# Kernel optimization log

Hardware: AMD Instinct MI355X
Metric: run time of the kernel (lower is better)

Reference implementation:

```python
import jax, jax.numpy as jnp
import numpy as np

N_NODES = 50000
N_EDGES = 800000
IN_FEATS = 128
OUT_FEATS = 128


def setup_inputs() -> dict:
    key = jax.random.key(0)
    k_feat, k_src, k_dst, k_w1, k_w2, k_lw = jax.random.split(key, 6)
    feat = jax.random.normal(k_feat, (N_NODES, IN_FEATS), dtype=jnp.float32)
    src_idx = jax.random.randint(k_src, (N_EDGES,), 0, N_NODES, dtype=jnp.int64 if jax.config.jax_enable_x64 else jnp.int32)
    dst_idx = jax.random.randint(k_dst, (N_EDGES,), 0, N_NODES, dtype=jnp.int64 if jax.config.jax_enable_x64 else jnp.int32)
    # xavier-uniform-ish scales
    w1_lim = float(np.sqrt(6.0 / (2 * IN_FEATS + IN_FEATS)))
    w2_lim = float(np.sqrt(6.0 / (IN_FEATS + OUT_FEATS)))
    lw_lim = float(np.sqrt(2.0) * np.sqrt(6.0 / (IN_FEATS + OUT_FEATS)))
    weight1 = jax.random.uniform(k_w1, (2 * IN_FEATS, IN_FEATS), jnp.float32, -w1_lim, w1_lim)
    weight2 = jax.random.uniform(k_w2, (IN_FEATS, OUT_FEATS), jnp.float32, -w2_lim, w2_lim)
    loop_weight = jax.random.uniform(k_lw, (IN_FEATS, OUT_FEATS), jnp.float32, -lw_lim, lw_lim)
    bias = jnp.zeros((OUT_FEATS,), dtype=jnp.float32)
    return {
        "feat": feat,
        "src_idx": src_idx,
        "dst_idx": dst_idx,
        "weight1": weight1,
        "weight2": weight2,
        "loop_weight": loop_weight,
        "bias": bias,
    }


def reference(feat, src_idx, dst_idx, weight1, weight2, loop_weight, bias):
    # Gather per-edge src/dst features and concat: [E, 2*d]
    feat_msg = jnp.concatenate([feat[src_idx], feat[dst_idx]], axis=-1)
    # 2-layer edge MLP: relu(msg @ W1) @ W2 -> [E, out]
    e_msg = jnp.matmul(jax.nn.relu(jnp.matmul(feat_msg, weight1)), weight2)
    # Scatter-sum to destination nodes: [N, out]
    rst = jax.ops.segment_sum(e_msg, dst_idx, num_segments=feat.shape[0])
    # bias + residual loop message
    rst = rst + bias + jnp.matmul(feat, loop_weight)
    return rst
```

## Files before the change

### kernel.cpp

```cpp
#include <hip/hip_runtime.h>

typedef __attribute__((ext_vector_type(8))) unsigned short ushort8v;
typedef __attribute__((ext_vector_type(8))) short short8v;
typedef __attribute__((ext_vector_type(4))) float f32x4;

__device__ inline unsigned short f2bf(float f) {
    union { float f; unsigned u; } v; v.f = f;
    unsigned u = v.u;
    unsigned r = (u + 0x7FFFu + ((u >> 16) & 1u)) >> 16;
    return (unsigned short)r;
}
__device__ inline float bf2f(unsigned short h) {
    union { unsigned u; float f; } v; v.u = ((unsigned)h) << 16;
    return v.f;
}

#define CAP 64

__global__ __launch_bounds__(256) void fused_pre(
    const float* __restrict__ feat, unsigned short* __restrict__ X2, int totalF,
    const float* __restrict__ W1, const float* __restrict__ W2,
    const float* __restrict__ LW,
    unsigned short* __restrict__ W1t, unsigned short* __restrict__ W3t,
    int cvtB) {
    int b = blockIdx.x, t = threadIdx.x;
    if (b < cvtB) {
        int idx = (b * 256 + t) * 4;
        if (idx >= totalF) return;
        float4 v = *(const float4*)(feat + idx);
        int row = idx >> 7, col = idx & 127;
        unsigned short* o = X2 + (size_t)row * 256 + 128 + col;
        *(ushort4*)o = make_ushort4(f2bf(v.x), f2bf(v.y), f2bf(v.z), f2bf(v.w));
    } else {
        int i = (b - cvtB) * 256 + t;
        if (i < 32768) {
            int jj = i >> 7, k = i & 127;
            float v = (jj < 128) ? W1[k * 128 + jj] : W1[(128 + k) * 128 + (jj - 128)];
            W1t[i] = f2bf(v);
        } else {
            int i2 = i - 32768;
            int n = i2 >> 8, k = i2 & 255;
            float v = (k < 128) ? W2[k * 128 + n] : LW[(k - 128) * 128 + n];
            W3t[i2] = f2bf(v);
        }
    }
}

template <bool OUT_BF16>
__device__ void gemm_tile(
    unsigned short* As, unsigned short* Bs,
    const unsigned short* __restrict__ A, int lda,
    const unsigned short* __restrict__ Bt, int ldb, int nRowsB,
    void* __restrict__ Cout, int ldc,
    const float* __restrict__ bias, int M, int K, int m0, int n0) {
    const int tid = threadIdx.x;
    const int lane = tid & 63;
    const int w = tid >> 6;
    const int wr = w >> 1, wc = w & 1;
    const int q = lane >> 4, ln = lane & 15;

    f32x4 acc[4][4];
#pragma unroll
    for (int i = 0; i < 4; i++)
#pragma unroll
        for (int j = 0; j < 4; j++) acc[i][j] = (f32x4)0.f;

    for (int kk = 0; kk < K; kk += 64) {
#pragma unroll
        for (int i = 0; i < 4; i++) {
            int id = i * 256 + tid;
            int r = id >> 3, b = id & 7;
            ushort8v v = (ushort8v)(unsigned short)0;
            int gr = m0 + r;
            if (gr < M) v = *(const ushort8v*)(A + (size_t)gr * lda + kk + b * 8);
            *(ushort8v*)(As + r * 64 + ((b ^ (r & 7)) * 8)) = v;
        }
#pragma unroll
        for (int i = 0; i < 4; i++) {
            int id = i * 256 + tid;
            int r = id >> 3, b = id & 7;
            ushort8v v = (ushort8v)(unsigned short)0;
            int gr = n0 + r;
            if (gr < nRowsB) v = *(const ushort8v*)(Bt + (size_t)gr * ldb + kk + b * 8);
            *(ushort8v*)(Bs + r * 64 + ((b ^ (r & 7)) * 8)) = v;
        }
        __syncthreads();
#pragma unroll
        for (int ks = 0; ks < 2; ks++) {
            short8v af[4], bfv[4];
#pragma unroll
            for (int ti = 0; ti < 4; ti++) {
                int m = wr * 64 + ti * 16 + ln;
                int blk = (ks * 4 + q) ^ (m & 7);
                af[ti] = *(const short8v*)(As + m * 64 + blk * 8);
            }
#pragma unroll
            for (int tj = 0; tj < 4; tj++) {
                int n = wc * 64 + tj * 16 + ln;
                int blk = (ks * 4 + q) ^ (n & 7);
                bfv[tj] = *(const short8v*)(Bs + n * 64 + blk * 8);
            }
#pragma unroll
            for (int ti = 0; ti < 4; ti++)
#pragma unroll
                for (int tj = 0; tj < 4; tj++)
                    acc[ti][tj] = __builtin_amdgcn_mfma_f32_16x16x32_bf16(
                        af[ti], bfv[tj], acc[ti][tj], 0, 0, 0);
        }
        __syncthreads();
    }

#pragma unroll
    for (int ti = 0; ti < 4; ti++) {
        int rowb = m0 + wr * 64 + ti * 16 + q * 4;
#pragma unroll
        for (int tj = 0; tj < 4; tj++) {
            int col = n0 + wc * 64 + tj * 16 + ln;
            f32x4 c = acc[ti][tj];
            float bv = 0.f;
            if (!OUT_BF16 && bias) bv = bias[col];
#pragma unroll
            for (int r = 0; r < 4; r++) {
                int row = rowb + r;
                if (row < M) {
                    if (OUT_BF16)
                        ((unsigned short*)Cout)[(size_t)row * ldc + col] = f2bf(c[r]);
                    else
                        ((float*)Cout)[(size_t)row * ldc + col] = c[r] + bv;
                }
            }
        }
    }
}

__global__ __launch_bounds__(256) void gemm1_scatter(
    const unsigned short* __restrict__ X2feat, const unsigned short* __restrict__ W1t,
    unsigned short* __restrict__ AB,
    const int* __restrict__ src, const int* __restrict__ dst,
    int* __restrict__ cur, int* __restrict__ eSrc,
    int E, int gemmB, int N) {
    __shared__ unsigned short smem[2 * 128 * 64];
    int b = blockIdx.x;
    int half = b >> 1;
    if ((b & 1) == 0) {
        if (half >= gemmB) return;
        int m0 = (half >> 1) * 128, n0 = (half & 1) * 128;
        gemm_tile<true>(smem, smem + 128 * 64, X2feat, 256, W1t, 128, 256,
                        (void*)AB, 256, nullptr, N, 128, m0, n0);
    } else {
        int e = (half * 256 + threadIdx.x) * 4;
        if (e + 3 < E) {
            int4 s4 = *(const int4*)(src + e);
            int4 d4 = *(const int4*)(dst + e);
            int p0 = atomicAdd(&cur[d4.x], 1);
            int p1 = atomicAdd(&cur[d4.y], 1);
            int p2 = atomicAdd(&cur[d4.z], 1);
            int p3 = atomicAdd(&cur[d4.w], 1);
            eSrc[(size_t)d4.x * CAP + min(p0, CAP - 1)] = s4.x;
            eSrc[(size_t)d4.y * CAP + min(p1, CAP - 1)] = s4.y;
            eSrc[(size_t)d4.z * CAP + min(p2, CAP - 1)] = s4.z;
            eSrc[(size_t)d4.w * CAP + min(p3, CAP - 1)] = s4.w;
        } else {
            for (int i = e; i < E && i >= 0; i++) {
                int d = dst[i];
                int pos = atomicAdd(&cur[d], 1);
                eSrc[(size_t)d * CAP + min(pos, CAP - 1)] = src[i];
            }
        }
    }
}

__global__ __launch_bounds__(256) void gather_kernel(
    const unsigned short* __restrict__ AB, const int* __restrict__ cur,
    const int* __restrict__ eSrc,
    unsigned short* __restrict__ X2, int N) {
    int wid = (blockIdx.x * 256 + threadIdx.x) >> 6;
    int lane = threadIdx.x & 63;
    if (wid >= N) return;
    int num = min(cur[wid], CAP);
    size_t start = (size_t)wid * CAP;
    int half = lane >> 5, ln32 = lane & 31;
    ushort4 bv = *(const ushort4*)(AB + (size_t)wid * 256 + 128 + ln32 * 4);
    float b0 = bf2f(bv.x), b1 = bf2f(bv.y), b2 = bf2f(bv.z), b3 = bf2f(bv.w);
    float p0 = 0.f, p1 = 0.f, p2 = 0.f, p3 = 0.f;

    int mySrc = (lane < num) ? eSrc[start + lane] : 0;
    int j = 0;
    for (; j + 8 <= num; j += 8) {
        ushort4 v[4];
#pragma unroll
        for (int u = 0; u < 4; u++) {
            int s = __shfl(mySrc, j + 2 * u + half);
            v[u] = *(const ushort4*)(AB + (size_t)s * 256 + ln32 * 4);
        }
#pragma unroll
        for (int u = 0; u < 4; u++) {
            p0 += fmaxf(bf2f(v[u].x) + b0, 0.f);
            p1 += fmaxf(bf2f(v[u].y) + b1, 0.f);
            p2 += fmaxf(bf2f(v[u].z) + b2, 0.f);
            p3 += fmaxf(bf2f(v[u].w) + b3, 0.f);
        }
    }
    for (; j < num; j += 2) {
        int idx = j + half;
        int s = __shfl(mySrc, idx);
        bool ok = idx < num;
        ushort4 v = *(const ushort4*)(AB + (size_t)s * 256 + ln32 * 4);
        float m = ok ? 1.f : 0.f;
        p0 += m * fmaxf(bf2f(v.x) + b0, 0.f);
        p1 += m * fmaxf(bf2f(v.y) + b1, 0.f);
        p2 += m * fmaxf(bf2f(v.z) + b2, 0.f);
        p3 += m * fmaxf(bf2f(v.w) + b3, 0.f);
    }
    p0 += __shfl_xor(p0, 32);
    p1 += __shfl_xor(p1, 32);
    p2 += __shfl_xor(p2, 32);
    p3 += __shfl_xor(p3, 32);
    if (half == 0) {
        *(ushort4*)(X2 + (size_t)wid * 256 + ln32 * 4) =
            make_ushort4(f2bf(p0), f2bf(p1), f2bf(p2), f2bf(p3));
    }
}

template <bool OUT_BF16>
__global__ __launch_bounds__(256) void gemm128(
    const unsigned short* __restrict__ A, int lda,
    const unsigned short* __restrict__ Bt, int ldb, int nRowsB,
    void* __restrict__ Cout, int ldc,
    const float* __restrict__ bias, int M, int K) {
    __shared__ unsigned short smem[2 * 128 * 64];
    gemm_tile<OUT_BF16>(smem, smem + 128 * 64, A, lda, Bt, ldb, nRowsB,
                        Cout, ldc, bias, M, K, blockIdx.x * 128, blockIdx.y * 128);
}

extern "C" void kernel_launch(void* const* d_in, const int* in_sizes, int n_in,
                              void* d_out, int out_size, void* d_ws, size_t ws_size,
                              hipStream_t stream) {
    const float* feat = (const float*)d_in[0];
    const int* src = (const int*)d_in[1];
    const int* dst = (const int*)d_in[2];
    const float* W1 = (const float*)d_in[3];
    const float* W2 = (const float*)d_in[4];
    const float* LW = (const float*)d_in[5];
    const float* bias = (const float*)d_in[6];
    float* out = (float*)d_out;

    const int N = in_sizes[0] / 128;
    const int E = in_sizes[1];

    char* ws = (char*)d_ws;
    unsigned short* X2 = (unsigned short*)ws;
    size_t off_b = (size_t)N * 256 * 2;
    unsigned short* AB = (unsigned short*)(ws + off_b);
    off_b += (size_t)N * 256 * 2;
    unsigned short* W1t = (unsigned short*)(ws + off_b);
    off_b += (size_t)256 * 128 * 2;
    unsigned short* W3t = (unsigned short*)(ws + off_b);
    off_b += (size_t)128 * 256 * 2;
    int* cur = (int*)(ws + off_b);   off_b += (size_t)N * 4;
    int* eSrc = (int*)(ws + off_b);  off_b += (size_t)N * CAP * 4;

    int totalF = N * 128;
    int cvtB = (totalF / 4 + 255) / 256;

    hipMemsetAsync(cur, 0, (size_t)N * 4, stream);
    fused_pre<<<cvtB + 256, 256, 0, stream>>>(
        feat, X2, totalF, W1, W2, LW, W1t, W3t, cvtB);

    int gemmB = ((N + 127) / 128) * 2;
    int scatB = ((E + 3) / 4 + 255) / 256;
    int mx = gemmB > scatB ? gemmB : scatB;
    gemm1_scatter<<<2 * mx, 256, 0, stream>>>(
        X2 + 128, W1t, AB, src, dst, cur, eSrc, E, gemmB, N);

    gather_kernel<<<(N + 3) / 4, 256, 0, stream>>>(AB, cur, eSrc, X2, N);

    dim3 g2((N + 127) / 128, 1);
    gemm128<false><<<g2, 256, 0, stream>>>(X2, 256, W3t, 256, 128,
                                           (void*)out, 128, bias, N, 256);
}
```

Baseline: 183.7 us.

## Split final GEMM: compute loop residual early, accumulate aggregated half later

The memset of the per-node counter array is folded into the preprocessing kernel as extra zeroing blocks, removing a separate memset launch. The self-loop GEMM (feat @ loop_weight + bias) now runs inside the gemm1/scatter kernel as extra even-indexed blocks, so it overlaps with the edge scatter and the first edge GEMM. The last kernel then does only a K=128 GEMM on the aggregated features and adds into the output with read-modify-write. This halves the K of the final GEMM but adds an extra read of the output and more blocks in the middle kernel.

```diff
diff --git a/kernel.cpp b/kernel.cpp
--- a/kernel.cpp
+++ b/kernel.cpp
@@ -22,7 +22,7 @@
     const float* __restrict__ W1, const float* __restrict__ W2,
     const float* __restrict__ LW,
     unsigned short* __restrict__ W1t, unsigned short* __restrict__ W3t,
-    int cvtB) {
+    int* __restrict__ cur, int N, int cvtB) {
     int b = blockIdx.x, t = threadIdx.x;
     if (b < cvtB) {
         int idx = (b * 256 + t) * 4;
@@ -31,7 +31,7 @@
         int row = idx >> 7, col = idx & 127;
         unsigned short* o = X2 + (size_t)row * 256 + 128 + col;
         *(ushort4*)o = make_ushort4(f2bf(v.x), f2bf(v.y), f2bf(v.z), f2bf(v.w));
-    } else {
+    } else if (b < cvtB + 256) {
         int i = (b - cvtB) * 256 + t;
         if (i < 32768) {
             int jj = i >> 7, k = i & 127;
@@ -43,10 +43,17 @@
             float v = (k < 128) ? W2[k * 128 + n] : LW[(k - 128) * 128 + n];
             W3t[i2] = f2bf(v);
         }
-    }
-}
-
-template <bool OUT_BF16>
+    } else {
+        int idx = ((b - cvtB - 256) * 256 + t) * 4;
+        if (idx + 3 < N) {
+            *(int4*)(cur + idx) = make_int4(0, 0, 0, 0);
+        } else {
+            for (int i = idx; i < N; i++) cur[i] = 0;
+        }
+    }
+}
+
+template <int OUT_MODE>
 __device__ void gemm_tile(
     unsigned short* As, unsigned short* Bs,
     const unsigned short* __restrict__ A, int lda,
@@ -118,13 +125,15 @@
             int col = n0 + wc * 64 + tj * 16 + ln;
             f32x4 c = acc[ti][tj];
             float bv = 0.f;
-            if (!OUT_BF16 && bias) bv = bias[col];
+            if (OUT_MODE == 0 && bias) bv = bias[col];
 #pragma unroll
             for (int r = 0; r < 4; r++) {
                 int row = rowb + r;
                 if (row < M) {
-                    if (OUT_BF16)
+                    if (OUT_MODE == 1)
                         ((unsigned short*)Cout)[(size_t)row * ldc + col] = f2bf(c[r]);
+                    else if (OUT_MODE == 2)
+                        ((float*)Cout)[(size_t)row * ldc + col] += c[r];
                     else
                         ((float*)Cout)[(size_t)row * ldc + col] = c[r] + bv;
                 }
@@ -135,18 +144,24 @@
 
 __global__ __launch_bounds__(256) void gemm1_scatter(
     const unsigned short* __restrict__ X2feat, const unsigned short* __restrict__ W1t,
-    unsigned short* __restrict__ AB,
+    const unsigned short* __restrict__ W3t, const float* __restrict__ bias,
+    unsigned short* __restrict__ AB, float* __restrict__ out,
     const int* __restrict__ src, const int* __restrict__ dst,
     int* __restrict__ cur, int* __restrict__ eSrc,
-    int E, int gemmB, int N) {
+    int E, int gemmB, int g2fB, int N) {
     __shared__ unsigned short smem[2 * 128 * 64];
     int b = blockIdx.x;
     int half = b >> 1;
     if ((b & 1) == 0) {
-        if (half >= gemmB) return;
-        int m0 = (half >> 1) * 128, n0 = (half & 1) * 128;
-        gemm_tile<true>(smem, smem + 128 * 64, X2feat, 256, W1t, 128, 256,
-                        (void*)AB, 256, nullptr, N, 128, m0, n0);
+        if (half < gemmB) {
+            int m0 = (half >> 1) * 128, n0 = (half & 1) * 128;
+            gemm_tile<1>(smem, smem + 128 * 64, X2feat, 256, W1t, 128, 256,
+                         (void*)AB, 256, nullptr, N, 128, m0, n0);
+        } else if (half < gemmB + g2fB) {
+            int m0 = (half - gemmB) * 128;
+            gemm_tile<0>(smem, smem + 128 * 64, X2feat, 256, W3t + 128, 256, 128,
+                         (void*)out, 128, bias, N, 128, m0, 0);
+        }
     } else {
         int e = (half * 256 + threadIdx.x) * 4;
         if (e + 3 < E) {
@@ -222,15 +237,12 @@
     }
 }
 
-template <bool OUT_BF16>
-__global__ __launch_bounds__(256) void gemm128(
-    const unsigned short* __restrict__ A, int lda,
-    const unsigned short* __restrict__ Bt, int ldb, int nRowsB,
-    void* __restrict__ Cout, int ldc,
-    const float* __restrict__ bias, int M, int K) {
+__global__ __launch_bounds__(256) void gemm_add(
+    const unsigned short* __restrict__ A, const unsigned short* __restrict__ W3t,
+    float* __restrict__ out, int N) {
     __shared__ unsigned short smem[2 * 128 * 64];
-    gemm_tile<OUT_BF16>(smem, smem + 128 * 64, A, lda, Bt, ldb, nRowsB,
-                        Cout, ldc, bias, M, K, blockIdx.x * 128, blockIdx.y * 128);
+    gemm_tile<2>(smem, smem + 128 * 64, A, 256, W3t, 256, 128,
+                 (void*)out, 128, nullptr, N, 128, blockIdx.x * 128, 0);
 }
 
 extern "C" void kernel_launch(void* const* d_in, const int* in_sizes, int n_in,
@@ -262,20 +274,21 @@
 
     int totalF = N * 128;
     int cvtB = (totalF / 4 + 255) / 256;
-
-    hipMemsetAsync(cur, 0, (size_t)N * 4, stream);
-    fused_pre<<<cvtB + 256, 256, 0, stream>>>(
-        feat, X2, totalF, W1, W2, LW, W1t, W3t, cvtB);
+    int zeroB = ((N + 3) / 4 + 255) / 256;
+
+    fused_pre<<<cvtB + 256 + zeroB, 256, 0, stream>>>(
+        feat, X2, totalF, W1, W2, LW, W1t, W3t, cur, N, cvtB);
 
     int gemmB = ((N + 127) / 128) * 2;
+    int g2fB = (N + 127) / 128;
     int scatB = ((E + 3) / 4 + 255) / 256;
-    int mx = gemmB > scatB ? gemmB : scatB;
+    int evenC = gemmB + g2fB;
+    int mx = evenC > scatB ? evenC : scatB;
     gemm1_scatter<<<2 * mx, 256, 0, stream>>>(
-        X2 + 128, W1t, AB, src, dst, cur, eSrc, E, gemmB, N);
+        X2 + 128, W1t, W3t, bias, AB, out, src, dst, cur, eSrc,
+        E, gemmB, g2fB, N);
 
     gather_kernel<<<(N + 3) / 4, 256, 0, stream>>>(AB, cur, eSrc, X2, N);
 
-    dim3 g2((N + 127) / 128, 1);
-    gemm128<false><<<g2, 256, 0, stream>>>(X2, 256, W3t, 256, 128,
-                                           (void*)out, 128, bias, N, 256);
-}
+    gemm_add<<<(N + 127) / 128, 256, 0, stream>>>(X2, W3t, out, N);
+}
```

Measured after the change: 195.0 us. 6.1% more time.
